# Performance work log

Hardware: AMD Instinct MI355X
Metric: run time of the kernel (lower is better)

## Reference

```python
import jax, jax.numpy as jnp
import numpy as np
from jax import lax

PATCH = 16
DILATIONS = (1, 2, 4, 8)
R2_THRESH = 0.5


def setup_inputs() -> dict:
    key = jax.random.key(0)
    k1, k2, k3 = jax.random.split(key, 3)
    seasonal = jax.random.normal(k1, (32, 2048, 8), dtype=jnp.float32)
    # 4 Conv1d(1,1,k=16) kernels + biases (PyTorch default init scale ~1/sqrt(k))
    conv_w = jax.random.normal(k2, (4, PATCH), dtype=jnp.float32) / np.sqrt(PATCH).astype(np.float32)
    conv_b = jax.random.normal(k3, (4,), dtype=jnp.float32) * 0.01
    return {"seasonal": seasonal, "conv_w": conv_w, "conv_b": conv_b}


def _r2(y):
    n = y.shape[-1]
    x = jnp.arange(n, dtype=y.dtype)
    xm = x - x.mean()                                  # [2p]
    ym = y - y.mean(axis=-1, keepdims=True)            # [..., 2p]
    sxy = jnp.einsum('...k,k->...', ym, xm)
    sxx = jnp.sum(xm * xm)
    syy = jnp.sum(ym * ym, axis=-1)
    return (sxy * sxy) / (sxx * syy)


def _forward(seasonal, conv_w, conv_b):
    B, S, C = seasonal.shape
    p = PATCH
    # channels are processed independently with the SAME convs -> fuse B and C
    x = seasonal.transpose(0, 2, 1).reshape(B * C, 1, S)  # [BC,1,S]
    win = jnp.arange(S - p + 1)[:, None] + jnp.arange(p)[None, :]  # [n_patches,p]
    cand_list = []
    for i, d in enumerate(DILATIONS):
        pad = (p - 1) * d
        out = lax.conv_general_dilated(
            x, conv_w[i].reshape(1, 1, p), window_strides=(1,),
            padding=[(pad, pad)], rhs_dilation=(d,)) + conv_b[i]
        out = out[:, 0, :S]                      # crop to seq_len, [BC,S]
        cand_list.append(out[:, win])            # sliding windows [BC,n_patches,p]
    cand = jnp.concatenate(cand_list, axis=1)    # [BC,N,p]
    N = cand.shape[1]

    # r^2 score for every adjacent pair (vectorized; greedy scan only gates it)
    pair = jnp.concatenate([cand[:, :-1], cand[:, 1:]], axis=-1)  # [BC,N-1,2p]
    can_merge = jnp.pad(_r2(pair) >= R2_THRESH, ((0, 0), (0, 1)),
                        constant_values=False)   # [BC,N]; last idx never merges

    # greedy sequential merge: if pair (i,i+1) merges, i+1 is consumed
    def step(consumed, cm_i):
        merge = jnp.logical_and(~consumed, cm_i)
        return merge, (merge, ~consumed)

    def scan_one(cm):
        _, (merge, valid) = lax.scan(step, jnp.zeros((), jnp.bool_), cm)
        return merge, valid

    merge, valid = jax.vmap(scan_one)(can_merge)  # [BC,N] each

    nxt = jnp.concatenate([cand[:, 1:], cand[:, -1:]], axis=1)
    outs = jnp.where(merge[..., None], 0.5 * (cand + nxt), cand)  # [BC,N,p]

    # pack selected patches to the front (stable order), zero-pad the tail
    order = jnp.argsort(~valid, axis=1)  # jax argsort is stable; valid first
    packed = jnp.take_along_axis(outs, order[..., None], axis=1)
    vmask = jnp.take_along_axis(valid, order, axis=1)
    packed = packed * vmask[..., None].astype(packed.dtype)

    return packed.reshape(B, C, N, p).transpose(0, 2, 3, 1)  # [B,N,p,C]


def reference(seasonal, conv_w, conv_b):
    return _forward(seasonal, conv_w, conv_b)
```

## Files before the change

kernel.cpp:

```cpp
#include <hip/hip_runtime.h>

#define SLEN 2048
#define PATCH 16
#define ND 4
#define NW 2033
#define NCAND 8132
#define NROWS 256
#define NCH 8
#define ROWPAD 8192


#define CDX(x) ((x) + ((x) >> 4))

__global__ __launch_bounds__(256) void k_convcm(
    const float* __restrict__ seasonal,
    const float* __restrict__ conv_w,
    const float* __restrict__ conv_b,
    float* __restrict__ convf,
    unsigned char* __restrict__ cmb)
{
    const int bid = blockIdx.x;
    const int row = bid >> 2;
    const int d   = bid & 3;
    const int dil = 1 << d;
    const int b = row >> 3, c = row & 7;
    const int tid = threadIdx.x;

    __shared__ float xs[SLEN];
    __shared__ double cd[CDX(SLEN-1)+1];

    #pragma unroll
    for (int j = 0; j < SLEN/256; ++j) {
        int s = tid + j*256;
        xs[s] = seasonal[(size_t)(b*SLEN + s)*NCH + c];
    }
    double w[PATCH];
    #pragma unroll
    for (int k = 0; k < PATCH; ++k) w[k] = (double)conv_w[d*PATCH + k];
    const double bias = (double)conv_b[d];
    __syncthreads();

    const size_t obase = (size_t)row*8192 + d*SLEN;
    #pragma unroll
    for (int j = 0; j < SLEN/256; ++j) {
        int t = tid + j*256;
        double acc = 0.0;
        #pragma unroll
        for (int k = 0; k < PATCH; ++k) {
            int idx = t - (PATCH-1-k)*dil;
            if (idx >= 0) acc += w[k] * (double)xs[idx];
        }
        acc += bias;
        cd[CDX(t)] = acc;
        convf[obase + t] = (float)acc;
    }
    __syncthreads();

    unsigned char* crow = cmb + (size_t)row*ROWPAD + d*NW;
    if (tid < 254) {
        const int w0 = tid*8;
        double W1=0.0, W2=0.0, Wk=0.0;
        #pragma unroll
        for (int k = 0; k < 16; ++k) {
            double v = cd[CDX(w0+k)];
            W1 += v; W2 = fma(v,v,W2); Wk = fma((double)k,v,Wk);
        }
        unsigned char bits[8];
        #pragma unroll
        for (int j = 0; j < 8; ++j) {
            double v0 = cd[CDX(w0+j)], v16 = cd[CDX(w0+j+16)];
            double nW1 = W1 + (v16 - v0);
            double nW2 = W2 + (v16*v16 - v0*v0);
            double nWk = Wk - W1 + v0 + 15.0*v16;
            double S1  = W1 + nW1;
            double S2  = W2 + nW2;
            double Sxy = (Wk - 15.5*W1) + (nWk + 0.5*nW1);
            double syy = S2 - S1*S1*(1.0/32.0);
            bits[j] = (unsigned char)((Sxy*Sxy >= 1364.0*syy) && (syy > 0.0));
            W1 = nW1; W2 = nW2; Wk = nWk;
        }
        #pragma unroll
        for (int j = 0; j < 8; ++j) crow[w0+j] = bits[j];
    } else if (tid == 255 && d < 3) {
        const int dil2 = dil << 1;
        double w2[PATCH];
        #pragma unroll
        for (int k = 0; k < PATCH; ++k) w2[k] = (double)conv_w[(d+1)*PATCH + k];
        const double bias2 = (double)conv_b[d+1];
        double aW1=0,aW2=0,aWk=0, bW1=0,bW2=0,bWk=0;
        #pragma unroll
        for (int k = 0; k < 16; ++k) {
            double va = cd[CDX(2032+k)];
            double acc = 0.0;
            #pragma unroll
            for (int q = 0; q < PATCH; ++q) {
                int idx = k - (PATCH-1-q)*dil2;
                if (idx >= 0) acc += w2[q] * (double)xs[idx];
            }
            double vb = acc + bias2;
            aW1 += va; aW2 = fma(va,va,aW2); aWk = fma((double)k,va,aWk);
            bW1 += vb; bW2 = fma(vb,vb,bW2); bWk = fma((double)k,vb,bWk);
        }
        double S1  = aW1 + bW1;
        double S2  = aW2 + bW2;
        double Sxy = (aWk - 15.5*aW1) + (bWk + 0.5*bW1);
        double syy = S2 - S1*S1*(1.0/32.0);
        crow[2032] = (unsigned char)((Sxy*Sxy >= 1364.0*syy) && (syy > 0.0));
    }
}

__global__ __launch_bounds__(256) void k_pack(
    const unsigned char* __restrict__ cmb,
    unsigned short* __restrict__ sel)
{
    const int row = blockIdx.x;
    const int tid = threadIdx.x;
    __shared__ unsigned char c0out[256];
    __shared__ int pmax[256];
    __shared__ unsigned sums[256];

    const unsigned* cmw = (const unsigned*)(cmb + (size_t)row*ROWPAD);
    unsigned cmbits = 0;
    #pragma unroll
    for (int q = 0; q < 8; ++q) {
        unsigned wrd = cmw[tid*8 + q];
        #pragma unroll
        for (int bb = 0; bb < 4; ++bb) {
            int p = tid*32 + q*4 + bb;
            unsigned bit = ((wrd >> (8*bb)) & 0xffu) ? 1u : 0u;
            if (p >= NCAND-1) bit = 0;
            cmbits |= bit << (q*4 + bb);
        }
    }

    unsigned inv = ~cmbits;
    unsigned T = (inv == 0u) ? 32u : (unsigned)__clz(inv);
    c0out[tid] = (unsigned char)(T & 1u);
    pmax[tid]  = (inv == 0u) ? -1 : tid;
    __syncthreads();
    for (int off = 1; off < 256; off <<= 1) {
        int v = (tid >= off) ? pmax[tid-off] : -1;
        __syncthreads();
        if (v > pmax[tid]) pmax[tid] = v;
        __syncthreads();
    }
    unsigned carry = 0;
    if (tid > 0) { int m = pmax[tid-1]; if (m >= 0) carry = c0out[m]; }

    unsigned cons = carry;
    unsigned validb = 0, mergeb = 0;
    int cnt = 0;
    const int base = tid*32;
    int nelem = NCAND - base; if (nelem > 32) nelem = 32; if (nelem < 0) nelem = 0;
    for (int w = 0; w < nelem; ++w) {
        unsigned bit = (cmbits >> w) & 1u;
        unsigned val = cons ^ 1u;
        unsigned mrg = bit & val;
        validb |= val << w;
        mergeb |= mrg << w;
        cnt += (int)val;
        cons = mrg;
    }

    sums[tid] = (unsigned)cnt;
    __syncthreads();
    for (int off = 1; off < 256; off <<= 1) {
        unsigned v = (tid >= off) ? sums[tid-off] : 0u;
        __syncthreads();
        sums[tid] += v;
        __syncthreads();
    }
    unsigned r = sums[tid] - (unsigned)cnt;
    unsigned total = sums[255];
    unsigned short* selrow = sel + (size_t)row*ROWPAD;
    for (int w = 0; w < nelem; ++w) {
        if ((validb >> w) & 1u)
            selrow[r++] = (unsigned short)((((base + w) << 1) | (int)((mergeb >> w) & 1u)));
    }
    for (int idx = (int)total + tid; idx < NCAND; idx += 256)
        selrow[idx] = 0xFFFFu;
}

__global__ __launch_bounds__(256) void k_out(
    const float* __restrict__ convf,
    const unsigned short* __restrict__ sel,
    float* __restrict__ out)
{
    __shared__ float gbuf[8*132];
    __shared__ int   amin_s[8], amax_s[8];
    __shared__ float tile[32*132];

    const int t = threadIdx.x;
    const int c = t & 7;
    const int s = t >> 3;
    const unsigned bq = blockIdx.x;
    const unsigned b  = bq / 255u;
    const unsigned m  = bq - b*255u;
    const int n0 = (int)m*32;
    const int ns = (NCAND - n0 < 32) ? (NCAND - n0) : 32;
    const unsigned row = b*NCH + (unsigned)c;

    if (t < 8) { amin_s[t] = 0x7fffffff; amax_s[t] = -1; }
    __syncthreads();

    int e = -1, ai = 0, ai2 = 0;
    if (s < ns) {
        unsigned short e16 = sel[(size_t)row*ROWPAD + (n0 + s)];
        e = (e16 == 0xFFFFu) ? -1 : (int)e16;
        if (e >= 0) {
            const int i  = e >> 1;
            const int d  = (i >= 3*NW) ? 3 : (i >= 2*NW) ? 2 : (i >= NW) ? 1 : 0;
            ai = i + 15*d;
            int ae;
            if (e & 1) {
                const int i2 = i + 1;
                const int d2 = (i2 >= 3*NW) ? 3 : (i2 >= 2*NW) ? 2 : (i2 >= NW) ? 1 : 0;
                ai2 = i2 + 15*d2;
                ae = ai2 + 16;
            } else {
                ai2 = ai;
                ae = ai + 16;
            }
            atomicMin(&amin_s[c], ai);
            atomicMax(&amax_s[c], ae);
        }
    }
    __syncthreads();

    {
        const int r = t >> 5, j = t & 31;
        const int lo = amin_s[r], hi = amax_s[r];
        if (lo <= hi) {
            const float* src = convf + (size_t)(b*NCH + r)*8192;
            for (int o = j; o <= hi - lo; o += 32)
                gbuf[r*132 + o] = src[lo + o];
        }
    }
    __syncthreads();

    float vals[16];
    if (e < 0) {
        #pragma unroll
        for (int k = 0; k < 16; ++k) vals[k] = 0.0f;
    } else {
        const float* f = gbuf + c*132 + (ai  - amin_s[c]);
        const float* g = gbuf + c*132 + (ai2 - amin_s[c]);
        if (e & 1) {
            #pragma unroll
            for (int k = 0; k < 16; ++k) vals[k] = 0.5f*(f[k] + g[k]);
        } else {
            #pragma unroll
            for (int k = 0; k < 16; ++k) vals[k] = f[k];
        }
    }
    if (s < ns) {
        float* tr = tile + s*132 + c;
        #pragma unroll
        for (int k = 0; k < 16; ++k) tr[k*8] = vals[k];
    }
    __syncthreads();

    const size_t obase = ((size_t)b*NCAND + n0)*128;
    const int nw = ns*128;
    #pragma unroll
    for (int m2 = 0; m2 < 4; ++m2) {
        int L = (t + m2*256)*4;
        if (L < nw) {
            int s2 = L >> 7, j = L & 127;
            float4 v = *(const float4*)&tile[s2*132 + j];
            *(float4*)&out[obase + L] = v;
        }
    }
}

extern "C" void kernel_launch(void* const* d_in, const int* in_sizes, int n_in,
                              void* d_out, int out_size, void* d_ws, size_t ws_size,
                              hipStream_t stream) {
    const float* seasonal = (const float*)d_in[0];
    const float* conv_w   = (const float*)d_in[1];
    const float* conv_b   = (const float*)d_in[2];
    float* out = (float*)d_out;

    char* ws = (char*)d_ws;
    unsigned short* sel   = (unsigned short*)(ws);
    float*          convf = (float*)(ws + 16777216);
    unsigned char*  cmb   = (unsigned char*)(ws + 25165824);

    hipLaunchKernelGGL(k_convcm, dim3(NROWS*ND), dim3(256), 0, stream,
                       seasonal, conv_w, conv_b, convf, cmb);
    hipLaunchKernelGGL(k_pack,   dim3(NROWS), dim3(256), 0, stream,
                       cmb, sel);
    hipLaunchKernelGGL(k_out,    dim3(32*255), dim3(256), 0, stream,
                       convf, sel, out);
}
```

Before: 171.1 us.

## Fuse conv, merge-flag and pack kernels into one per-row block

Merges the conv/merge-flag kernel and the pack kernel into a single 512-thread kernel per row. All four dilations are computed in shared memory, and each thread produces four outputs from register-cached inputs. Merge flags stay in shared memory instead of making a global round trip. The LDS-based scans are replaced with wave shuffle scans. This removes a kernel launch and the global cmb traffic, but drops to 256 blocks, which lowers parallelism across CUs and raises LDS use per block.

Measured after the change: 161.9 us. 5.3% less time.

```diff
diff --git a/kernel.cpp b/kernel.cpp
--- a/kernel.cpp
+++ b/kernel.cpp
@@ -11,173 +11,201 @@
 
 
 #define CDX(x) ((x) + ((x) >> 4))
-
-__global__ __launch_bounds__(256) void k_convcm(
+#define XSX(x) ((x) + ((x) >> 3))
+
+__global__ __launch_bounds__(512) void k1(
     const float* __restrict__ seasonal,
     const float* __restrict__ conv_w,
     const float* __restrict__ conv_b,
     float* __restrict__ convf,
-    unsigned char* __restrict__ cmb)
-{
-    const int bid = blockIdx.x;
-    const int row = bid >> 2;
-    const int d   = bid & 3;
-    const int dil = 1 << d;
-    const int b = row >> 3, c = row & 7;
-    const int tid = threadIdx.x;
-
-    __shared__ float xs[SLEN];
-    __shared__ double cd[CDX(SLEN-1)+1];
-
-    #pragma unroll
-    for (int j = 0; j < SLEN/256; ++j) {
-        int s = tid + j*256;
-        xs[s] = seasonal[(size_t)(b*SLEN + s)*NCH + c];
-    }
-    double w[PATCH];
-    #pragma unroll
-    for (int k = 0; k < PATCH; ++k) w[k] = (double)conv_w[d*PATCH + k];
-    const double bias = (double)conv_b[d];
-    __syncthreads();
-
-    const size_t obase = (size_t)row*8192 + d*SLEN;
-    #pragma unroll
-    for (int j = 0; j < SLEN/256; ++j) {
-        int t = tid + j*256;
-        double acc = 0.0;
-        #pragma unroll
-        for (int k = 0; k < PATCH; ++k) {
-            int idx = t - (PATCH-1-k)*dil;
-            if (idx >= 0) acc += w[k] * (double)xs[idx];
-        }
-        acc += bias;
-        cd[CDX(t)] = acc;
-        convf[obase + t] = (float)acc;
-    }
-    __syncthreads();
-
-    unsigned char* crow = cmb + (size_t)row*ROWPAD + d*NW;
-    if (tid < 254) {
-        const int w0 = tid*8;
-        double W1=0.0, W2=0.0, Wk=0.0;
-        #pragma unroll
-        for (int k = 0; k < 16; ++k) {
-            double v = cd[CDX(w0+k)];
-            W1 += v; W2 = fma(v,v,W2); Wk = fma((double)k,v,Wk);
-        }
-        unsigned char bits[8];
-        #pragma unroll
-        for (int j = 0; j < 8; ++j) {
-            double v0 = cd[CDX(w0+j)], v16 = cd[CDX(w0+j+16)];
-            double nW1 = W1 + (v16 - v0);
-            double nW2 = W2 + (v16*v16 - v0*v0);
-            double nWk = Wk - W1 + v0 + 15.0*v16;
-            double S1  = W1 + nW1;
-            double S2  = W2 + nW2;
-            double Sxy = (Wk - 15.5*W1) + (nWk + 0.5*nW1);
-            double syy = S2 - S1*S1*(1.0/32.0);
-            bits[j] = (unsigned char)((Sxy*Sxy >= 1364.0*syy) && (syy > 0.0));
-            W1 = nW1; W2 = nW2; Wk = nWk;
-        }
-        #pragma unroll
-        for (int j = 0; j < 8; ++j) crow[w0+j] = bits[j];
-    } else if (tid == 255 && d < 3) {
-        const int dil2 = dil << 1;
-        double w2[PATCH];
-        #pragma unroll
-        for (int k = 0; k < PATCH; ++k) w2[k] = (double)conv_w[(d+1)*PATCH + k];
-        const double bias2 = (double)conv_b[d+1];
-        double aW1=0,aW2=0,aWk=0, bW1=0,bW2=0,bWk=0;
-        #pragma unroll
-        for (int k = 0; k < 16; ++k) {
-            double va = cd[CDX(2032+k)];
-            double acc = 0.0;
-            #pragma unroll
-            for (int q = 0; q < PATCH; ++q) {
-                int idx = k - (PATCH-1-q)*dil2;
-                if (idx >= 0) acc += w2[q] * (double)xs[idx];
-            }
-            double vb = acc + bias2;
-            aW1 += va; aW2 = fma(va,va,aW2); aWk = fma((double)k,va,aWk);
-            bW1 += vb; bW2 = fma(vb,vb,bW2); bWk = fma((double)k,vb,bWk);
-        }
-        double S1  = aW1 + bW1;
-        double S2  = aW2 + bW2;
-        double Sxy = (aWk - 15.5*aW1) + (bWk + 0.5*bW1);
-        double syy = S2 - S1*S1*(1.0/32.0);
-        crow[2032] = (unsigned char)((Sxy*Sxy >= 1364.0*syy) && (syy > 0.0));
-    }
-}
-
-__global__ __launch_bounds__(256) void k_pack(
-    const unsigned char* __restrict__ cmb,
     unsigned short* __restrict__ sel)
 {
     const int row = blockIdx.x;
+    const int b = row >> 3, c = row & 7;
     const int tid = threadIdx.x;
-    __shared__ unsigned char c0out[256];
-    __shared__ int pmax[256];
-    __shared__ unsigned sums[256];
-
-    const unsigned* cmw = (const unsigned*)(cmb + (size_t)row*ROWPAD);
+
+    __shared__ float  xs[XSX(SLEN-1)+1];
+    __shared__ double cd[CDX(ND*SLEN-1)+1];
+    __shared__ unsigned char c0s[512];
+    __shared__ int      wmax[8];
+    __shared__ unsigned wsum[8];
+
+    for (int j = tid; j < SLEN; j += 512)
+        xs[XSX(j)] = seasonal[(size_t)(b*SLEN + j)*NCH + c];
+    __syncthreads();
+
+    for (int d = 0; d < ND; ++d) {
+        const int dil = 1 << d;
+        double w[PATCH];
+        #pragma unroll
+        for (int k = 0; k < PATCH; ++k) w[k] = (double)conv_w[d*PATCH + k];
+        const double bias = (double)conv_b[d];
+        const int r  = tid & (dil - 1);
+        const int g  = tid >> d;
+        const int bx = g*4*dil + r;
+
+        double xt[19];
+        #pragma unroll
+        for (int q = 0; q < 19; ++q) {
+            int idx = bx + (q - 15)*dil;
+            xt[q] = (idx >= 0) ? (double)xs[XSX(idx)] : 0.0;
+        }
+        double acc[4];
+        #pragma unroll
+        for (int m = 0; m < 4; ++m) acc[m] = 0.0;
+        if (g >= 4) {
+            #pragma unroll
+            for (int m = 0; m < 4; ++m)
+                #pragma unroll
+                for (int k = 0; k < PATCH; ++k)
+                    acc[m] += w[k] * xt[m + k];
+        } else {
+            #pragma unroll
+            for (int m = 0; m < 4; ++m)
+                #pragma unroll
+                for (int k = 0; k < PATCH; ++k)
+                    if (4*g + m + k - 15 >= 0)
+                        acc[m] += w[k] * xt[m + k];
+        }
+        const int ob = d*SLEN + bx;
+        #pragma unroll
+        for (int m = 0; m < 4; ++m)
+            cd[CDX(ob + m*dil)] = acc[m] + bias;
+    }
+    __syncthreads();
+
+    {
+        float* dst = convf + (size_t)row * ROWPAD;
+        #pragma unroll
+        for (int j = 0; j < 4; ++j) {
+            int i4 = (tid + j*512) * 4;
+            float4 v;
+            v.x = (float)cd[CDX(i4+0)];
+            v.y = (float)cd[CDX(i4+1)];
+            v.z = (float)cd[CDX(i4+2)];
+            v.w = (float)cd[CDX(i4+3)];
+            *(float4*)&dst[i4] = v;
+        }
+    }
+
+    unsigned char* cmL = (unsigned char*)xs;
+    {
+        const int d  = tid >> 7;
+        const int u  = tid & 127;
+        const int db = d * SLEN;
+        if (u < 127) {
+            const int w0 = u * 16;
+            double W1=0.0, W2=0.0, Wk=0.0;
+            #pragma unroll
+            for (int k = 0; k < 16; ++k) {
+                double v = cd[CDX(db + w0 + k)];
+                W1 += v; W2 = fma(v,v,W2); Wk = fma((double)k,v,Wk);
+            }
+            unsigned char* crow = cmL + d*NW;
+            #pragma unroll
+            for (int j = 0; j < 16; ++j) {
+                double v0 = cd[CDX(db+w0+j)], v16 = cd[CDX(db+w0+j+16)];
+                double nW1 = W1 + (v16 - v0);
+                double nW2 = W2 + (v16*v16 - v0*v0);
+                double nWk = Wk - W1 + v0 + 15.0*v16;
+                double S1  = W1 + nW1;
+                double S2  = W2 + nW2;
+                double Sxy = (Wk - 15.5*W1) + (nWk + 0.5*nW1);
+                double syy = S2 - S1*S1*(1.0/32.0);
+                crow[w0+j] = (unsigned char)((Sxy*Sxy >= 1364.0*syy) && (syy > 0.0));
+                W1 = nW1; W2 = nW2; Wk = nWk;
+            }
+        } else if (d < 3) {
+            double aW1=0,aW2=0,aWk=0, bW1=0,bW2=0,bWk=0;
+            #pragma unroll
+            for (int k = 0; k < 16; ++k) {
+                double va = cd[CDX(db + 2032 + k)];
+                double vb = cd[CDX(db + SLEN + k)];
+                aW1 += va; aW2 = fma(va,va,aW2); aWk = fma((double)k,va,aWk);
+                bW1 += vb; bW2 = fma(vb,vb,bW2); bWk = fma((double)k,vb,bWk);
+            }
+            double S1  = aW1 + bW1;
+            double S2  = aW2 + bW2;
+            double Sxy = (aWk - 15.5*aW1) + (bWk + 0.5*bW1);
+            double syy = S2 - S1*S1*(1.0/32.0);
+            cmL[d*NW + 2032] = (unsigned char)((Sxy*Sxy >= 1364.0*syy) && (syy > 0.0));
+        }
+        if (tid < 61) cmL[NCAND - 1 + tid] = 0;
+    }
+    __syncthreads();
+
+    const int base = tid * 16;
     unsigned cmbits = 0;
-    #pragma unroll
-    for (int q = 0; q < 8; ++q) {
-        unsigned wrd = cmw[tid*8 + q];
-        #pragma unroll
-        for (int bb = 0; bb < 4; ++bb) {
-            int p = tid*32 + q*4 + bb;
-            unsigned bit = ((wrd >> (8*bb)) & 0xffu) ? 1u : 0u;
-            if (p >= NCAND-1) bit = 0;
-            cmbits |= bit << (q*4 + bb);
-        }
-    }
-
-    unsigned inv = ~cmbits;
-    unsigned T = (inv == 0u) ? 32u : (unsigned)__clz(inv);
-    c0out[tid] = (unsigned char)(T & 1u);
-    pmax[tid]  = (inv == 0u) ? -1 : tid;
-    __syncthreads();
-    for (int off = 1; off < 256; off <<= 1) {
-        int v = (tid >= off) ? pmax[tid-off] : -1;
-        __syncthreads();
-        if (v > pmax[tid]) pmax[tid] = v;
-        __syncthreads();
-    }
-    unsigned carry = 0;
-    if (tid > 0) { int m = pmax[tid-1]; if (m >= 0) carry = c0out[m]; }
-
-    unsigned cons = carry;
-    unsigned validb = 0, mergeb = 0;
+    {
+        const unsigned* cw = (const unsigned*)cmL;
+        #pragma unroll
+        for (int q = 0; q < 4; ++q) {
+            unsigned wrd = cw[tid*4 + q];
+            #pragma unroll
+            for (int bb = 0; bb < 4; ++bb) {
+                unsigned bit = ((wrd >> (8*bb)) & 0xffu) ? 1u : 0u;
+                cmbits |= bit << (q*4 + bb);
+            }
+        }
+    }
+    unsigned inv16 = (~cmbits) & 0xffffu;
+    const bool allones = (inv16 == 0u);
+    unsigned T = allones ? 16u : (unsigned)__clz(inv16 << 16);
+    c0s[tid] = (unsigned char)(T & 1u);
+    int pm = allones ? -1 : tid;
+
+    const int lane = tid & 63, wid = tid >> 6;
+    int mscan = pm;
+    #pragma unroll
+    for (int off = 1; off < 64; off <<= 1) {
+        int v = __shfl_up(mscan, off);
+        if (lane >= off && v > mscan) mscan = v;
+    }
+    if (lane == 63) wmax[wid] = mscan;
+    __syncthreads();
+    int pshift = __shfl_up(mscan, 1);
+    int mexcl = (lane == 0) ? -1 : pshift;
+    #pragma unroll
+    for (int wq = 0; wq < 8; ++wq)
+        if (wq < wid) { int v = wmax[wq]; if (v > mexcl) mexcl = v; }
+    unsigned carry = (mexcl >= 0) ? (unsigned)c0s[mexcl] : 0u;
+
+    int nelem = NCAND - base; if (nelem > 16) nelem = 16; if (nelem < 0) nelem = 0;
+    unsigned cons = carry, validb = 0, mergeb = 0;
     int cnt = 0;
-    const int base = tid*32;
-    int nelem = NCAND - base; if (nelem > 32) nelem = 32; if (nelem < 0) nelem = 0;
-    for (int w = 0; w < nelem; ++w) {
-        unsigned bit = (cmbits >> w) & 1u;
+    for (int w2 = 0; w2 < nelem; ++w2) {
+        unsigned bit = (cmbits >> w2) & 1u;
         unsigned val = cons ^ 1u;
         unsigned mrg = bit & val;
-        validb |= val << w;
-        mergeb |= mrg << w;
+        validb |= val << w2;
+        mergeb |= mrg << w2;
         cnt += (int)val;
         cons = mrg;
     }
 
-    sums[tid] = (unsigned)cnt;
-    __syncthreads();
-    for (int off = 1; off < 256; off <<= 1) {
-        unsigned v = (tid >= off) ? sums[tid-off] : 0u;
-        __syncthreads();
-        sums[tid] += v;
-        __syncthreads();
-    }
-    unsigned r = sums[tid] - (unsigned)cnt;
-    unsigned total = sums[255];
-    unsigned short* selrow = sel + (size_t)row*ROWPAD;
-    for (int w = 0; w < nelem; ++w) {
-        if ((validb >> w) & 1u)
-            selrow[r++] = (unsigned short)((((base + w) << 1) | (int)((mergeb >> w) & 1u)));
-    }
-    for (int idx = (int)total + tid; idx < NCAND; idx += 256)
+    int sscan = cnt;
+    #pragma unroll
+    for (int off = 1; off < 64; off <<= 1) {
+        int v = __shfl_up(sscan, off);
+        if (lane >= off) sscan += v;
+    }
+    if (lane == 63) wsum[wid] = (unsigned)sscan;
+    __syncthreads();
+    unsigned wbase = 0, total = 0;
+    #pragma unroll
+    for (int wq = 0; wq < 8; ++wq) {
+        unsigned v = wsum[wq];
+        if (wq < wid) wbase += v;
+        total += v;
+    }
+    unsigned r = wbase + (unsigned)(sscan - cnt);
+
+    unsigned short* selrow = sel + (size_t)row * ROWPAD;
+    for (int w2 = 0; w2 < nelem; ++w2) {
+        if ((validb >> w2) & 1u)
+            selrow[r++] = (unsigned short)(((base + w2) << 1) | (int)((mergeb >> w2) & 1u));
+    }
+    for (int idx = (int)total + tid; idx < NCAND; idx += 512)
         selrow[idx] = 0xFFFFu;
 }
 
@@ -284,12 +312,9 @@
     char* ws = (char*)d_ws;
     unsigned short* sel   = (unsigned short*)(ws);
     float*          convf = (float*)(ws + 16777216);
-    unsigned char*  cmb   = (unsigned char*)(ws + 25165824);
-
-    hipLaunchKernelGGL(k_convcm, dim3(NROWS*ND), dim3(256), 0, stream,
-                       seasonal, conv_w, conv_b, convf, cmb);
-    hipLaunchKernelGGL(k_pack,   dim3(NROWS), dim3(256), 0, stream,
-                       cmb, sel);
-    hipLaunchKernelGGL(k_out,    dim3(32*255), dim3(256), 0, stream,
+
+    hipLaunchKernelGGL(k1,    dim3(NROWS), dim3(512), 0, stream,
+                       seasonal, conv_w, conv_b, convf, sel);
+    hipLaunchKernelGGL(k_out, dim3(32*255), dim3(256), 0, stream,
                        convf, sel, out);
 }
```
